# Kernel optimization log

Hardware: AMD Instinct MI355X
Metric: run time of the kernel (lower is better)

## Reference

```python
import jax, jax.numpy as jnp
import numpy as np
from functools import partial

# CUBA LIF/LI constants (from init_kwargs / hxtorch CUBALIFParams defaults)
DT = 1e-6
TAU_MEM = 8e-6
TAU_SYN = 8e-6
DV = DT / TAU_MEM  # 0.125 membrane integration factor
DI = DT / TAU_SYN  # 0.125 synaptic decay factor
ALPHA = 50.0       # SuperSpike surrogate sharpness
THRESHOLD = 1.0    # spike threshold (leak = reset = 0)


@partial(jax.custom_vjp, nondiff_argnums=(1,))
def superspike(x, alpha):
    # Heaviside forward, SuperSpike surrogate backward
    return (x > 0.0).astype(x.dtype)

def _ss_fwd(x, alpha):
    return superspike(x, alpha), x

def _ss_bwd(alpha, x, g):
    return (g / (alpha * jnp.abs(x) + 1.0) ** 2,)

superspike.defvjp(_ss_fwd, _ss_bwd)


def setup_inputs() -> dict:
    key = jax.random.key(0)
    k1, k2, k3 = jax.random.split(key, 3)
    T, B, N_IN, N_H, N_OUT = 512, 128, 256, 1024, 32
    # Bernoulli(0.1) input spike trains (0/1 floats)
    spikes = (jax.random.uniform(k1, (T, B, N_IN)) < 0.1).astype(jnp.float32)
    w_h = jax.random.normal(k2, (N_H, N_IN), jnp.float32) * 0.1
    w_o = jax.random.normal(k3, (N_OUT, N_H), jnp.float32) * 0.05
    return {"spikes": spikes, "w_h": w_h, "w_o": w_o}


def _lif_scan(c):
    # c: [T, B, H] synaptic input currents; returns spike trace z: [T, B, H]
    B, H = c.shape[1], c.shape[2]
    def step(carry, c_t):
        v, i = carry
        i = i * (1.0 - DI) + c_t                 # synaptic current decay + input
        v = v + DV * (i - v)                      # membrane leaky integration (leak=0)
        z = superspike(v - THRESHOLD, ALPHA)      # spike
        zd = jax.lax.stop_gradient(z)
        v = (1.0 - zd) * v                        # reset to 0 (detached spike)
        return (v, i), z
    init = (jnp.zeros((B, H), c.dtype), jnp.zeros((B, H), c.dtype))
    _, z = jax.lax.scan(step, init, c)
    return z


def _li_scan(c):
    # c: [T, B, O]; returns membrane trace v: [T, B, O] (no spike/reset)
    B, O = c.shape[1], c.shape[2]
    def step(carry, c_t):
        v, i = carry
        i = i * (1.0 - DI) + c_t
        v = v + DV * (i - v)
        return (v, i), v
    init = (jnp.zeros((B, O), c.dtype), jnp.zeros((B, O), c.dtype))
    _, v = jax.lax.scan(step, init, c)
    return v


def reference(spikes, w_h, w_o):
    # hidden synapse: dense projection for all timesteps at once
    c_h = jnp.einsum('tbi,hi->tbh', spikes, w_h)
    # hidden CUBA LIF layer (sequential recurrence over time)
    z_h = _lif_scan(c_h)
    # output synapse
    c_o = jnp.einsum('tbh,oh->tbo', z_h, w_o)
    # readout CUBA LI layer -> membrane trace [T, B, n_out]
    return _li_scan(c_o)
```

## Files before the change

kernel.cpp:

```cpp
#include <hip/hip_runtime.h>
#include <stdint.h>

#define T_STEPS 512
#define BATCH   128
#define N_IN    256
#define N_H     1024
#define N_OUT   32

typedef __attribute__((ext_vector_type(2))) float f32x2;

#define WS_WIDE_NEEDED 22282240u

template<int WIDE>
__global__ __launch_bounds__(256) void k_prep(const float* __restrict__ spikes,
                                              uint32_t* __restrict__ pm,
                                              uint16_t* __restrict__ pt,
                                              uint32_t* __restrict__ cnts) {
    __shared__ uint16_t list[64];
    __shared__ uint32_t wcnt[4];
    const int tid = threadIdx.x;
    const int wave = tid >> 6, lane = tid & 63;
    for (int r = 0; r < 4; ++r) {
        const int row = blockIdx.x * 4 + r;
        float s = spikes[(size_t)row * N_IN + tid];
        bool act = s > 0.5f;
        unsigned long long m = __ballot(act);
        if (tid < 64) list[tid] = 256;
        if (lane == 0) wcnt[wave] = (uint32_t)__popcll(m);
        __syncthreads();
        uint32_t off = 0;
        for (int w = 0; w < wave; ++w) off += wcnt[w];
        uint32_t total = wcnt[0] + wcnt[1] + wcnt[2] + wcnt[3];
        if (act) {
            uint32_t pos = off + (uint32_t)__popcll(m & ((1ull << lane) - 1ull));
            if (pos < 64) list[pos] = (uint16_t)tid;
        }
        __syncthreads();
        if (WIDE) {
            if (tid < 32) {
                int h = tid >> 4, sl = tid & 15;
                pm[(uint32_t)row * 32 + tid] = ((uint32_t)list[2 * sl + h]) << 8;
            } else if (tid < 64) {
                int u = tid & 31;
                int h = u >> 4, sl = u & 15;
                pt[(uint32_t)row * 32 + u] = list[32 + 2 * sl + h];
            }
        } else {
            if (tid < 32) {
                int w = tid;
                int g = w >> 3;
                int jl = (2 * w) & 15;
                int srcb = (g >> 1) * 32 + (g & 1);
                uint32_t lo = list[srcb + 2 * jl];
                uint32_t hi = list[srcb + 2 * (jl + 1)];
                pm[(uint32_t)row * 32 + w] = lo | (hi << 16);
            }
        }
        if (tid == 0) cnts[row] = total < 64u ? total : 64u;
        __syncthreads();
    }
}

__global__ __launch_bounds__(256) void k_tr(const float* __restrict__ w_h,
                                            float* __restrict__ w_t) {
    int gid = blockIdx.x * 256 + threadIdx.x;
    int h = gid >> 8, i = gid & 255;
    w_t[(size_t)i * N_H + h] = w_h[gid];
}

__device__ __forceinline__ float xadd32(float x) {
    float a = x, b = x;
    asm("v_permlane32_swap_b32 %0, %1" : "+v"(a), "+v"(b));
    return a + b;
}

struct IdxSet { uint4 a, b, c, d; };

template<int WIDE>
__global__ __launch_bounds__(256) void k_lif(const uint32_t* __restrict__ pm,
                                             const uint16_t* __restrict__ pt,
                                             const uint32_t* __restrict__ cnts,
                                             const float* __restrict__ w_t,
                                             uint32_t* __restrict__ zmask) {
    extern __shared__ __align__(16) float wl[];
    const int bg = blockIdx.x >> 4, tile = blockIdx.x & 15;
    const int h0 = tile * 64, tid = threadIdx.x;

    #pragma unroll 8
    for (int k = 0; k < 16; ++k) {
        int idx = (k << 8) + tid;
        int i = idx >> 4, c4 = (idx & 15) << 2;
        *(float4*)(wl + i * 64 + c4) =
            *(const float4*)(w_t + (size_t)i * N_H + h0 + c4);
    }
    if (tid < 64) wl[256 * 64 + tid] = 0.0f;
    __syncthreads();

    const int wv = __builtin_amdgcn_readfirstlane(tid >> 6);
    const int b  = (bg << 2) + wv;
    const int l  = tid & 63;
    const int duo2 = (l & 31) << 1;
    const int half16 = (l >> 5) << 4;
    const int half32 = (l >> 5) << 4;
    const char* wlb = (const char*)wl + (duo2 << 2);

    int vzero;
    asm("v_mov_b32 %0, 0" : "=v"(vzero));

    uint32_t cW0, cW1, cW2, cW3;
    IdxSet W0, W1, W2, W3;

#define LOADSET(CN, S, ROW) { \
    uint32_t ro_ = (uint32_t)(ROW); \
    CN = *(cnts + ro_ + vzero); \
    if (WIDE) { \
        const uint4* mp_ = (const uint4*)(pm + ro_ * 32u + half32); \
        S.a = mp_[0]; S.b = mp_[1]; S.c = mp_[2]; S.d = mp_[3]; \
    } else { \
        const uint4* mp_ = (const uint4*)(pt + ro_ * 64u + half16); \
        S.a = mp_[0]; S.b = mp_[1]; \
    } }

#define GCHUNK4(G, Q) { \
    G += *(const f32x2*)(wlb + (Q).x); \
    G += *(const f32x2*)(wlb + (Q).y); \
    G += *(const f32x2*)(wlb + (Q).z); \
    G += *(const f32x2*)(wlb + (Q).w); }

#define GCHUNK2(G, U0, U1) { \
    uint32_t ia0 = (U0) & 0xFFFFu; \
    uint32_t ia1 = (U0) >> 16; \
    uint32_t ia2 = (U1) & 0xFFFFu; \
    uint32_t ia3 = (U1) >> 16; \
    G += *(const f32x2*)(wl + ia0 * 64 + duo2); \
    G += *(const f32x2*)(wl + ia1 * 64 + duo2); \
    G += *(const f32x2*)(wl + ia2 * 64 + duo2); \
    G += *(const f32x2*)(wl + ia3 * 64 + duo2); }

#define GATHER_MAIN(G, S) { \
    if (WIDE) { GCHUNK4(G, S.a) GCHUNK4(G, S.b) GCHUNK4(G, S.c) GCHUNK4(G, S.d) } \
    else { GCHUNK2(G, S.a.x, S.a.y) GCHUNK2(G, S.a.z, S.a.w) \
           GCHUNK2(G, S.b.x, S.b.y) GCHUNK2(G, S.b.z, S.b.w) } }

#define GATHER_TAIL(G, CN, ROW) do { \
    uint32_t cs = __builtin_amdgcn_readfirstlane(CN); \
    if (cs > 32u) { \
        uint32_t ro_ = (uint32_t)(ROW); \
        const uint4* tp = WIDE ? (const uint4*)(pt + ro_ * 32u + half16) \
                               : (const uint4*)(pt + ro_ * 64u + 32u + half16); \
        uint4 T0 = tp[0], T1 = tp[1]; \
        GCHUNK2(G, T0.x, T0.y) \
        if (cs > 40u) GCHUNK2(G, T0.z, T0.w) \
        if (cs > 48u) GCHUNK2(G, T1.x, T1.y) \
        if (cs > 56u) GCHUNK2(G, T1.z, T1.w) \
    } } while (0)

#define SCANSTEP(G, ROW) { \
    float c0 = xadd32(G.x); \
    float c1 = xadd32(G.y); \
    s0 = __builtin_fmaf(s0, 0.875f, c0); \
    s1 = __builtin_fmaf(s1, 0.875f, c1); \
    v0 = __builtin_fmaf(0.125f, s0 - v0, v0); \
    v1 = __builtin_fmaf(0.125f, s1 - v1, v1); \
    unsigned long long m0 = __ballot(v0 > 1.0f); \
    unsigned long long m1 = __ballot(v1 > 1.0f); \
    if (v0 > 1.0f) v0 = 0.0f; \
    if (v1 > 1.0f) v1 = 0.0f; \
    if (l == 0) { \
        uint2* zp = (uint2*)(zmask + (uint32_t)((ROW) * 32 + (tile << 1))); \
        *zp = make_uint2((uint32_t)m0, (uint32_t)m1); } }

    float v0 = 0, v1 = 0, s0 = 0, s1 = 0;
    LOADSET(cW0, W0, b);
    LOADSET(cW1, W1, BATCH + b);
    LOADSET(cW2, W2, 2 * BATCH + b);
    LOADSET(cW3, W3, 3 * BATCH + b);

    for (int t = 0; t < T_STEPS; t += 4) {
        const int rowA = t * BATCH + b;
        const int rowB = rowA + BATCH;
        const int rowC = rowB + BATCH;
        const int rowD = rowC + BATCH;

        f32x2 ga = {0.0f, 0.0f}, gb = {0.0f, 0.0f};
        GATHER_MAIN(ga, W0);
        GATHER_MAIN(gb, W1);
        GATHER_TAIL(ga, cW0, rowA);
        GATHER_TAIL(gb, cW1, rowB);
        {
            int r4 = t + 4; if (r4 > T_STEPS - 1) r4 = T_STEPS - 1;
            int r5 = t + 5; if (r5 > T_STEPS - 1) r5 = T_STEPS - 1;
            LOADSET(cW0, W0, r4 * BATCH + b);
            LOADSET(cW1, W1, r5 * BATCH + b);
        }
        SCANSTEP(ga, rowA);
        SCANSTEP(gb, rowB);

        f32x2 gc = {0.0f, 0.0f}, gd = {0.0f, 0.0f};
        GATHER_MAIN(gc, W2);
        GATHER_MAIN(gd, W3);
        GATHER_TAIL(gc, cW2, rowC);
        GATHER_TAIL(gd, cW3, rowD);
        {
            int r6 = t + 6; if (r6 > T_STEPS - 1) r6 = T_STEPS - 1;
            int r7 = t + 7; if (r7 > T_STEPS - 1) r7 = T_STEPS - 1;
            LOADSET(cW2, W2, r6 * BATCH + b);
            LOADSET(cW3, W3, r7 * BATCH + b);
        }
        SCANSTEP(gc, rowC);
        SCANSTEP(gd, rowD);
    }
#undef LOADSET
#undef GCHUNK4
#undef GCHUNK2
#undef GATHER_MAIN
#undef GATHER_TAIL
#undef SCANSTEP
}

#define DPP_TERM(X, CTRL) \
    __int_as_float(__builtin_amdgcn_update_dpp(0, __float_as_int(X), CTRL, 0xF, 0xF, true))

__global__ __launch_bounds__(256) void k_li(const uint32_t* __restrict__ zmask,
                                            const float* __restrict__ w_o,
                                            float* __restrict__ out,
                                            float2* __restrict__ svbuf) {
    extern __shared__ __align__(16) float wo[];
    const int gb  = blockIdx.x;
    const int seg = gb >> 9;
    const int rem = gb & 511;
    const int b   = rem >> 2;
    const int oct = rem & 3;
    const int o0  = oct << 3;
    const int tid = threadIdx.x;
    for (int lin = tid; lin < 8 * 1024; lin += 256) {
        int ol = lin >> 10, idx = lin & 1023;
        int word = idx >> 5, j = idx & 31;
        int h = ((word >> 1) << 6) + (j << 1) + (word & 1);
        wo[ol * 1025 + idx] = w_o[(size_t)(o0 + ol) * N_H + h];
    }
    __syncthreads();

    const int ol = tid >> 5, word = tid & 31;
    const float* wrow = wo + ol * 1025 + (word << 5);
    const int t0 = seg << 7, t1 = t0 + 128;

    float v = 0.0f, s = 0.0f;
    uint32_t mA = zmask[(size_t)(t0 * BATCH + b) * 32 + word];
    uint32_t mB = zmask[(size_t)((t0 + 1) * BATCH + b) * 32 + word];
    for (int t = t0; t < t1; t += 2) {
        uint32_t ma = mA, mb = mB;
        int ta = (t + 2 < t1) ? t + 2 : t;
        int tb = (t + 3 < t1) ? t + 3 : t;
        mA = zmask[(size_t)(ta * BATCH + b) * 32 + word];
        mB = zmask[(size_t)(tb * BATCH + b) * 32 + word];

        float c0 = 0.0f, c1 = 0.0f;
        while (ma) { int j = __builtin_ctz(ma); ma &= ma - 1; c0 += wrow[j]; }
        while (mb) { int j = __builtin_ctz(mb); mb &= mb - 1; c1 += wrow[j]; }

        c0 += DPP_TERM(c0, 0x111);  c1 += DPP_TERM(c1, 0x111);
        c0 += DPP_TERM(c0, 0x112);  c1 += DPP_TERM(c1, 0x112);
        c0 += DPP_TERM(c0, 0x114);  c1 += DPP_TERM(c1, 0x114);
        c0 += DPP_TERM(c0, 0x118);  c1 += DPP_TERM(c1, 0x118);
        c0 += DPP_TERM(c0, 0x142);  c1 += DPP_TERM(c1, 0x142);

        s = __builtin_fmaf(s, 0.875f, c0);
        v = __builtin_fmaf(0.125f, s - v, v);
        if (word == 31)
            out[(size_t)(t * BATCH + b) * 32 + o0 + ol] = v;

        s = __builtin_fmaf(s, 0.875f, c1);
        v = __builtin_fmaf(0.125f, s - v, v);
        if (word == 31)
            out[(size_t)((t + 1) * BATCH + b) * 32 + o0 + ol] = v;
    }
    if (word == 31)
        svbuf[((size_t)seg * BATCH + b) * 32 + o0 + ol] = make_float2(s, v);
}

__global__ __launch_bounds__(256) void k_fix(const float2* __restrict__ svbuf,
                                             float* __restrict__ out) {
    int idx = blockIdx.x * 256 + threadIdx.x;
    int o = idx & 31;
    int r = idx >> 5;
    int b = r & 127;
    int t = 128 + (r >> 7);
    int seg = t >> 7;
    int k = (t & 127) + 1;
    const float A128 = 3.7714379e-8f;
    const float C128 = 6.0343007e-7f;
    float2 S = svbuf[(size_t)b * 32 + o];
    if (seg >= 2) {
        float2 z = svbuf[((size_t)BATCH + b) * 32 + o];
        S = make_float2(z.x + A128 * S.x, z.y + A128 * S.y + C128 * S.x);
    }
    if (seg >= 3) {
        float2 z = svbuf[((size_t)2 * BATCH + b) * 32 + o];
        S = make_float2(z.x + A128 * S.x, z.y + A128 * S.y + C128 * S.x);
    }
    float ak = exp2f((float)k * -0.19264508f);
    float corr = __builtin_fmaf(ak, S.y, 0.125f * (float)k * ak * S.x);
    out[(size_t)(t * BATCH + b) * 32 + o] += corr;
}

extern "C" void kernel_launch(void* const* d_in, const int* in_sizes, int n_in,
                              void* d_out, int out_size, void* d_ws, size_t ws_size,
                              hipStream_t stream) {
    const float* spikes = (const float*)d_in[0];
    const float* w_h    = (const float*)d_in[1];
    const float* w_o    = (const float*)d_in[2];
    float* out = (float*)d_out;

    char* ws = (char*)d_ws;
    const int lds12 = (256 * 64 + 64) * 4;
    const int lds34 = 8 * 1025 * 4;

    if (ws_size >= WS_WIDE_NEEDED) {
        uint32_t* pm    = (uint32_t*)(ws);
        uint16_t* pt    = (uint16_t*)(ws + 8388608);
        uint32_t* cnts  = (uint32_t*)(ws + 12582912);
        float*    w_t   = (float*)   (ws + 12845056);
        uint32_t* zmask = (uint32_t*)(ws + 13893632);
        float2*   svbuf = (float2*)  (ws);

        hipFuncSetAttribute((const void*)k_lif<1>, hipFuncAttributeMaxDynamicSharedMemorySize, lds12);
        hipFuncSetAttribute((const void*)k_li,     hipFuncAttributeMaxDynamicSharedMemorySize, lds34);

        k_prep<1><<<(T_STEPS * BATCH) / 4, 256, 0, stream>>>(spikes, pm, pt, cnts);
        k_tr<<<(N_H * N_IN) / 256, 256, 0, stream>>>(w_h, w_t);
        k_lif<1><<<512, 256, lds12, stream>>>(pm, pt, cnts, w_t, zmask);
        k_li<<<4 * BATCH * 4, 256, lds34, stream>>>(zmask, w_o, out, svbuf);
        k_fix<<<(384 * BATCH * N_OUT) / 256, 256, 0, stream>>>(svbuf, out);
    } else {
        uint32_t* pairs = (uint32_t*)(ws);
        uint32_t* cnts  = (uint32_t*)(ws + 8388608);
        float*    w_t   = (float*)   (ws + 8650752);
        uint32_t* zmask = (uint32_t*)(ws + 9699328);
        float2*   svbuf = (float2*)  (ws);

        hipFuncSetAttribute((const void*)k_lif<0>, hipFuncAttributeMaxDynamicSharedMemorySize, lds12);
        hipFuncSetAttribute((const void*)k_li,     hipFuncAttributeMaxDynamicSharedMemorySize, lds34);

        k_prep<0><<<(T_STEPS * BATCH) / 4, 256, 0, stream>>>(spikes, pairs, (uint16_t*)pairs, cnts);
        k_tr<<<(N_H * N_IN) / 256, 256, 0, stream>>>(w_h, w_t);
        k_lif<0><<<512, 256, lds12, stream>>>(pairs, (const uint16_t*)pairs, cnts, w_t, zmask);
        k_li<<<4 * BATCH * 4, 256, lds34, stream>>>(zmask, w_o, out, svbuf);
        k_fix<<<(384 * BATCH * N_OUT) / 256, 256, 0, stream>>>(svbuf, out);
    }
}
```

Baseline: 431.9 us.

## Narrow LIF hidden tile to 32 columns and double the block grid

The LIF kernel now gives each block 32 hidden neurons instead of 64, so it launches 1024 blocks instead of 512. Each lane handles one neuron instead of a pair of neurons loaded as float2. The LDS weight tile shrinks by half, the index scaling and zmask layout are changed to match, and the k_li weight permutation becomes a straight copy. The aim is more parallelism and occupancy in the latency-bound sequential scan. In exchange, every block repeats the index loads and the cross-lane reduction for half as much work. The fallback path for a smaller workspace is also removed.

```diff
diff --git a/kernel.cpp b/kernel.cpp
--- a/kernel.cpp
+++ b/kernel.cpp
@@ -9,9 +9,7 @@
 
 typedef __attribute__((ext_vector_type(2))) float f32x2;
 
-#define WS_WIDE_NEEDED 22282240u
-
-template<int WIDE>
+
 __global__ __launch_bounds__(256) void k_prep(const float* __restrict__ spikes,
                                               uint32_t* __restrict__ pm,
                                               uint16_t* __restrict__ pt,
@@ -36,25 +34,13 @@
             if (pos < 64) list[pos] = (uint16_t)tid;
         }
         __syncthreads();
-        if (WIDE) {
-            if (tid < 32) {
-                int h = tid >> 4, sl = tid & 15;
-                pm[(uint32_t)row * 32 + tid] = ((uint32_t)list[2 * sl + h]) << 8;
-            } else if (tid < 64) {
-                int u = tid & 31;
-                int h = u >> 4, sl = u & 15;
-                pt[(uint32_t)row * 32 + u] = list[32 + 2 * sl + h];
-            }
-        } else {
-            if (tid < 32) {
-                int w = tid;
-                int g = w >> 3;
-                int jl = (2 * w) & 15;
-                int srcb = (g >> 1) * 32 + (g & 1);
-                uint32_t lo = list[srcb + 2 * jl];
-                uint32_t hi = list[srcb + 2 * (jl + 1)];
-                pm[(uint32_t)row * 32 + w] = lo | (hi << 16);
-            }
+        if (tid < 32) {
+            int h = tid >> 4, sl = tid & 15;
+            pm[(uint32_t)row * 32 + tid] = ((uint32_t)list[2 * sl + h]) << 7;
+        } else if (tid < 64) {
+            int u = tid & 31;
+            int h = u >> 4, sl = u & 15;
+            pt[(uint32_t)row * 32 + u] = list[32 + 2 * sl + h];
         }
         if (tid == 0) cnts[row] = total < 64u ? total : 64u;
         __syncthreads();
@@ -76,33 +62,31 @@
 
 struct IdxSet { uint4 a, b, c, d; };
 
-template<int WIDE>
 __global__ __launch_bounds__(256) void k_lif(const uint32_t* __restrict__ pm,
                                              const uint16_t* __restrict__ pt,
                                              const uint32_t* __restrict__ cnts,
                                              const float* __restrict__ w_t,
                                              uint32_t* __restrict__ zmask) {
     extern __shared__ __align__(16) float wl[];
-    const int bg = blockIdx.x >> 4, tile = blockIdx.x & 15;
-    const int h0 = tile * 64, tid = threadIdx.x;
+    const int bg = blockIdx.x >> 5, tile = blockIdx.x & 31;
+    const int h0 = tile * 32, tid = threadIdx.x;
 
     #pragma unroll 8
-    for (int k = 0; k < 16; ++k) {
+    for (int k = 0; k < 8; ++k) {
         int idx = (k << 8) + tid;
-        int i = idx >> 4, c4 = (idx & 15) << 2;
-        *(float4*)(wl + i * 64 + c4) =
+        int i = idx >> 3, c4 = (idx & 7) << 2;
+        *(float4*)(wl + i * 32 + c4) =
             *(const float4*)(w_t + (size_t)i * N_H + h0 + c4);
     }
-    if (tid < 64) wl[256 * 64 + tid] = 0.0f;
+    if (tid < 32) wl[256 * 32 + tid] = 0.0f;
     __syncthreads();
 
     const int wv = __builtin_amdgcn_readfirstlane(tid >> 6);
     const int b  = (bg << 2) + wv;
     const int l  = tid & 63;
-    const int duo2 = (l & 31) << 1;
-    const int half16 = (l >> 5) << 4;
+    const int col = l & 31;
     const int half32 = (l >> 5) << 4;
-    const char* wlb = (const char*)wl + (duo2 << 2);
+    const char* wlb = (const char*)wl + (col << 2);
 
     int vzero;
     asm("v_mov_b32 %0, 0" : "=v"(vzero));
@@ -113,64 +97,49 @@
 #define LOADSET(CN, S, ROW) { \
     uint32_t ro_ = (uint32_t)(ROW); \
     CN = *(cnts + ro_ + vzero); \
-    if (WIDE) { \
-        const uint4* mp_ = (const uint4*)(pm + ro_ * 32u + half32); \
-        S.a = mp_[0]; S.b = mp_[1]; S.c = mp_[2]; S.d = mp_[3]; \
-    } else { \
-        const uint4* mp_ = (const uint4*)(pt + ro_ * 64u + half16); \
-        S.a = mp_[0]; S.b = mp_[1]; \
-    } }
+    const uint4* mp_ = (const uint4*)(pm + ro_ * 32u + half32); \
+    S.a = mp_[0]; S.b = mp_[1]; S.c = mp_[2]; S.d = mp_[3]; }
 
 #define GCHUNK4(G, Q) { \
-    G += *(const f32x2*)(wlb + (Q).x); \
-    G += *(const f32x2*)(wlb + (Q).y); \
-    G += *(const f32x2*)(wlb + (Q).z); \
-    G += *(const f32x2*)(wlb + (Q).w); }
-
-#define GCHUNK2(G, U0, U1) { \
+    G += *(const float*)(wlb + (Q).x); \
+    G += *(const float*)(wlb + (Q).y); \
+    G += *(const float*)(wlb + (Q).z); \
+    G += *(const float*)(wlb + (Q).w); }
+
+#define GATHER_MAIN(G, S) { \
+    GCHUNK4(G, S.a) GCHUNK4(G, S.b) GCHUNK4(G, S.c) GCHUNK4(G, S.d) }
+
+#define GTCHUNK(G, U0, U1) { \
     uint32_t ia0 = (U0) & 0xFFFFu; \
     uint32_t ia1 = (U0) >> 16; \
     uint32_t ia2 = (U1) & 0xFFFFu; \
     uint32_t ia3 = (U1) >> 16; \
-    G += *(const f32x2*)(wl + ia0 * 64 + duo2); \
-    G += *(const f32x2*)(wl + ia1 * 64 + duo2); \
-    G += *(const f32x2*)(wl + ia2 * 64 + duo2); \
-    G += *(const f32x2*)(wl + ia3 * 64 + duo2); }
-
-#define GATHER_MAIN(G, S) { \
-    if (WIDE) { GCHUNK4(G, S.a) GCHUNK4(G, S.b) GCHUNK4(G, S.c) GCHUNK4(G, S.d) } \
-    else { GCHUNK2(G, S.a.x, S.a.y) GCHUNK2(G, S.a.z, S.a.w) \
-           GCHUNK2(G, S.b.x, S.b.y) GCHUNK2(G, S.b.z, S.b.w) } }
+    G += *(wl + ia0 * 32 + col); \
+    G += *(wl + ia1 * 32 + col); \
+    G += *(wl + ia2 * 32 + col); \
+    G += *(wl + ia3 * 32 + col); }
 
 #define GATHER_TAIL(G, CN, ROW) do { \
     uint32_t cs = __builtin_amdgcn_readfirstlane(CN); \
     if (cs > 32u) { \
         uint32_t ro_ = (uint32_t)(ROW); \
-        const uint4* tp = WIDE ? (const uint4*)(pt + ro_ * 32u + half16) \
-                               : (const uint4*)(pt + ro_ * 64u + 32u + half16); \
+        const uint4* tp = (const uint4*)(pt + ro_ * 32u + half32); \
         uint4 T0 = tp[0], T1 = tp[1]; \
-        GCHUNK2(G, T0.x, T0.y) \
-        if (cs > 40u) GCHUNK2(G, T0.z, T0.w) \
-        if (cs > 48u) GCHUNK2(G, T1.x, T1.y) \
-        if (cs > 56u) GCHUNK2(G, T1.z, T1.w) \
+        GTCHUNK(G, T0.x, T0.y) \
+        if (cs > 40u) GTCHUNK(G, T0.z, T0.w) \
+        if (cs > 48u) GTCHUNK(G, T1.x, T1.y) \
+        if (cs > 56u) GTCHUNK(G, T1.z, T1.w) \
     } } while (0)
 
 #define SCANSTEP(G, ROW) { \
-    float c0 = xadd32(G.x); \
-    float c1 = xadd32(G.y); \
-    s0 = __builtin_fmaf(s0, 0.875f, c0); \
-    s1 = __builtin_fmaf(s1, 0.875f, c1); \
+    float c = xadd32(G); \
+    s0 = __builtin_fmaf(s0, 0.875f, c); \
     v0 = __builtin_fmaf(0.125f, s0 - v0, v0); \
-    v1 = __builtin_fmaf(0.125f, s1 - v1, v1); \
-    unsigned long long m0 = __ballot(v0 > 1.0f); \
-    unsigned long long m1 = __ballot(v1 > 1.0f); \
+    unsigned long long m = __ballot(v0 > 1.0f); \
     if (v0 > 1.0f) v0 = 0.0f; \
-    if (v1 > 1.0f) v1 = 0.0f; \
-    if (l == 0) { \
-        uint2* zp = (uint2*)(zmask + (uint32_t)((ROW) * 32 + (tile << 1))); \
-        *zp = make_uint2((uint32_t)m0, (uint32_t)m1); } }
-
-    float v0 = 0, v1 = 0, s0 = 0, s1 = 0;
+    if (l == 0) zmask[(uint32_t)((ROW) * 32 + tile)] = (uint32_t)m; }
+
+    float v0 = 0, s0 = 0;
     LOADSET(cW0, W0, b);
     LOADSET(cW1, W1, BATCH + b);
     LOADSET(cW2, W2, 2 * BATCH + b);
@@ -182,7 +151,7 @@
         const int rowC = rowB + BATCH;
         const int rowD = rowC + BATCH;
 
-        f32x2 ga = {0.0f, 0.0f}, gb = {0.0f, 0.0f};
+        float ga = 0.0f, gb = 0.0f;
         GATHER_MAIN(ga, W0);
         GATHER_MAIN(gb, W1);
         GATHER_TAIL(ga, cW0, rowA);
@@ -196,7 +165,7 @@
         SCANSTEP(ga, rowA);
         SCANSTEP(gb, rowB);
 
-        f32x2 gc = {0.0f, 0.0f}, gd = {0.0f, 0.0f};
+        float gc = 0.0f, gd = 0.0f;
         GATHER_MAIN(gc, W2);
         GATHER_MAIN(gd, W3);
         GATHER_TAIL(gc, cW2, rowC);
@@ -212,8 +181,8 @@
     }
 #undef LOADSET
 #undef GCHUNK4
-#undef GCHUNK2
 #undef GATHER_MAIN
+#undef GTCHUNK
 #undef GATHER_TAIL
 #undef SCANSTEP
 }
@@ -235,9 +204,7 @@
     const int tid = threadIdx.x;
     for (int lin = tid; lin < 8 * 1024; lin += 256) {
         int ol = lin >> 10, idx = lin & 1023;
-        int word = idx >> 5, j = idx & 31;
-        int h = ((word >> 1) << 6) + (j << 1) + (word & 1);
-        wo[ol * 1025 + idx] = w_o[(size_t)(o0 + ol) * N_H + h];
+        wo[ol * 1025 + idx] = w_o[(size_t)(o0 + ol) * N_H + idx];
     }
     __syncthreads();
 
@@ -313,39 +280,21 @@
     float* out = (float*)d_out;
 
     char* ws = (char*)d_ws;
-    const int lds12 = (256 * 64 + 64) * 4;
+    uint32_t* pm    = (uint32_t*)(ws);
+    uint16_t* pt    = (uint16_t*)(ws + 8388608);
+    uint32_t* cnts  = (uint32_t*)(ws + 12582912);
+    float*    w_t   = (float*)   (ws + 12845056);
+    uint32_t* zmask = (uint32_t*)(ws + 13893632);
+    float2*   svbuf = (float2*)  (ws);
+
+    const int lds12 = (256 * 32 + 32) * 4;
     const int lds34 = 8 * 1025 * 4;
-
-    if (ws_size >= WS_WIDE_NEEDED) {
-        uint32_t* pm    = (uint32_t*)(ws);
-        uint16_t* pt    = (uint16_t*)(ws + 8388608);
-        uint32_t* cnts  = (uint32_t*)(ws + 12582912);
-        float*    w_t   = (float*)   (ws + 12845056);
-        uint32_t* zmask = (uint32_t*)(ws + 13893632);
-        float2*   svbuf = (float2*)  (ws);
-
-        hipFuncSetAttribute((const void*)k_lif<1>, hipFuncAttributeMaxDynamicSharedMemorySize, lds12);
-        hipFuncSetAttribute((const void*)k_li,     hipFuncAttributeMaxDynamicSharedMemorySize, lds34);
-
-        k_prep<1><<<(T_STEPS * BATCH) / 4, 256, 0, stream>>>(spikes, pm, pt, cnts);
-        k_tr<<<(N_H * N_IN) / 256, 256, 0, stream>>>(w_h, w_t);
-        k_lif<1><<<512, 256, lds12, stream>>>(pm, pt, cnts, w_t, zmask);
-        k_li<<<4 * BATCH * 4, 256, lds34, stream>>>(zmask, w_o, out, svbuf);
-        k_fix<<<(384 * BATCH * N_OUT) / 256, 256, 0, stream>>>(svbuf, out);
-    } else {
-        uint32_t* pairs = (uint32_t*)(ws);
-        uint32_t* cnts  = (uint32_t*)(ws + 8388608);
-        float*    w_t   = (float*)   (ws + 8650752);
-        uint32_t* zmask = (uint32_t*)(ws + 9699328);
-        float2*   svbuf = (float2*)  (ws);
-
-        hipFuncSetAttribute((const void*)k_lif<0>, hipFuncAttributeMaxDynamicSharedMemorySize, lds12);
-        hipFuncSetAttribute((const void*)k_li,     hipFuncAttributeMaxDynamicSharedMemorySize, lds34);
-
-        k_prep<0><<<(T_STEPS * BATCH) / 4, 256, 0, stream>>>(spikes, pairs, (uint16_t*)pairs, cnts);
-        k_tr<<<(N_H * N_IN) / 256, 256, 0, stream>>>(w_h, w_t);
-        k_lif<0><<<512, 256, lds12, stream>>>(pairs, (const uint16_t*)pairs, cnts, w_t, zmask);
-        k_li<<<4 * BATCH * 4, 256, lds34, stream>>>(zmask, w_o, out, svbuf);
-        k_fix<<<(384 * BATCH * N_OUT) / 256, 256, 0, stream>>>(svbuf, out);
-    }
-}
+    hipFuncSetAttribute((const void*)k_lif, hipFuncAttributeMaxDynamicSharedMemorySize, lds12);
+    hipFuncSetAttribute((const void*)k_li,  hipFuncAttributeMaxDynamicSharedMemorySize, lds34);
+
+    k_prep<<<(T_STEPS * BATCH) / 4, 256, 0, stream>>>(spikes, pm, pt, cnts);
+    k_tr<<<(N_H * N_IN) / 256, 256, 0, stream>>>(w_h, w_t);
+    k_lif<<<32 * 32, 256, lds12, stream>>>(pm, pt, cnts, w_t, zmask);
+    k_li<<<4 * BATCH * 4, 256, lds34, stream>>>(zmask, w_o, out, svbuf);
+    k_fix<<<(384 * BATCH * N_OUT) / 256, 256, 0, stream>>>(svbuf, out);
+}
```

New measurement: 532.8 us. 1.23x slower.
